# Optimization experiments

Hardware: AMD Instinct MI355X
Metric: run time of the kernel (lower is better)

## Reference

```python
import jax, jax.numpy as jnp
import numpy as np

EPS = 1e-6

def layernorm2d(x, w, b):
    # x: [B,C,H,W]; normalize over channel dim per spatial location
    mu = jnp.mean(x, axis=1, keepdims=True)
    var = jnp.var(x, axis=1, keepdims=True)
    xn = (x - mu) / jnp.sqrt(var + EPS)
    return xn * w[None, :, None, None] + b[None, :, None, None]

def mish(x):
    return x * jnp.tanh(jax.nn.softplus(x))

def setup_inputs() -> dict:
    key = jax.random.key(0)
    ks = jax.random.split(key, 16)
    B, C, H, W, T = 16, 192, 96, 96, 512
    s = 0.02
    return {
        "t": jax.random.normal(ks[0], (B, T), jnp.float32),
        "x_l": jax.random.normal(ks[1], (B, C, H, W), jnp.float32),
        "x_r": jax.random.normal(ks[2], (B, C, H, W), jnp.float32),
        "ln_wl": jnp.ones((C,), jnp.float32),
        "ln_bl": jnp.zeros((C,), jnp.float32),
        "ln_wr": jnp.ones((C,), jnp.float32),
        "ln_br": jnp.zeros((C,), jnp.float32),
        "Wl1": jax.random.normal(ks[3], (C, C), jnp.float32) * s,
        "bl1": jnp.zeros((C,), jnp.float32),
        "Wr1": jax.random.normal(ks[4], (C, C), jnp.float32) * s,
        "br1": jnp.zeros((C,), jnp.float32),
        "Wl2": jax.random.normal(ks[5], (C, C), jnp.float32) * s,
        "bl2": jnp.zeros((C,), jnp.float32),
        "Wr2": jax.random.normal(ks[6], (C, C), jnp.float32) * s,
        "br2": jnp.zeros((C,), jnp.float32),
        "beta": jnp.zeros((C,), jnp.float32),
        "gamma": jnp.zeros((C,), jnp.float32),
        "Wt": jax.random.normal(ks[7], (C, T), jnp.float32) * s,
        "bt": jnp.zeros((C,), jnp.float32),
    }

def reference(t, x_l, x_r, ln_wl, ln_bl, ln_wr, ln_br,
              Wl1, bl1, Wr1, br1, Wl2, bl2, Wr2, br2,
              beta, gamma, Wt, bt):
    C = x_l.shape[1]
    scale = C ** (-0.5)
    # 1x1 convs as channel einsums; outputs in bhwc layout
    Q_l = jnp.einsum('bchw,oc->bhwo', layernorm2d(x_l, ln_wl, ln_bl), Wl1) + bl1  # [B,H,Wl,C]
    Q_r = jnp.einsum('bchw,oc->bhwo', layernorm2d(x_r, ln_wr, ln_br), Wr1) + br1  # [B,H,Wr,C]
    V_l = jnp.einsum('bchw,oc->bhwo', x_l, Wl2) + bl2
    V_r = jnp.einsum('bchw,oc->bhwo', x_r, Wr2) + br2
    att = jnp.einsum('bhxc,bhyc->bhxy', Q_l, Q_r) * scale  # [B,H,Wl,Wr]
    F_r2l = jnp.einsum('bhxy,bhyc->bhxc', jax.nn.softmax(att, axis=-1), V_r)
    F_l2r = jnp.einsum('bhxy,bhxc->bhyc', jax.nn.softmax(att, axis=2), V_l)
    temb = (mish(t) @ Wt.T + bt)[:, :, None, None]  # [B,C,1,1]
    out_l = x_l + jnp.transpose(F_r2l, (0, 3, 1, 2)) * beta[None, :, None, None] + temb
    out_r = x_r + jnp.transpose(F_l2r, (0, 3, 1, 2)) * gamma[None, :, None, None] + temb
    return (out_l, out_r)
```

## Files before the change

kernel.cpp:

```cpp
#include <hip/hip_runtime.h>


typedef __attribute__((ext_vector_type(8))) short bhalf8;
typedef __attribute__((ext_vector_type(4))) float f32x4;

#define DEVI static __device__ __forceinline__

constexpr int Cc   = 192;
constexpr int HWc  = 9216;
constexpr int CHW  = 192 * 9216;
constexpr int HALF_OUT = 16 * CHW;

DEVI unsigned short f2bf(float f) {
  unsigned u = __builtin_bit_cast(unsigned, f);
  u += 0x7fffu + ((u >> 16) & 1u);
  return (unsigned short)(u >> 16);
}
DEVI float bf2f(unsigned short h) {
  unsigned u = (unsigned)h << 16;
  return __builtin_bit_cast(float, u);
}
DEVI float bf2f_s(short h) { return bf2f((unsigned short)h); }

__global__ void setup1(
    const float* __restrict__ t,
    const float* __restrict__ lnwl, const float* __restrict__ lnbl,
    const float* __restrict__ lnwr, const float* __restrict__ lnbr,
    const float* __restrict__ Wl1, const float* __restrict__ bl1,
    const float* __restrict__ Wr1, const float* __restrict__ br1,
    const float* __restrict__ Wl2, const float* __restrict__ Wr2,
    short* __restrict__ W1l_b, short* __restrict__ W1r_b,
    short* __restrict__ W2l_b, short* __restrict__ W2r_b,
    float* __restrict__ s1l, float* __restrict__ t1l,
    float* __restrict__ s1r, float* __restrict__ t1r,
    float* __restrict__ mt)
{
  const int blk = blockIdx.x, tid = threadIdx.x;
  if (blk < 576) {
    int id  = blk * 256 + tid;
    int m   = id / 36864;
    int rem = id - m * 36864;
    int c   = rem % 192;
    float v;
    short* dst;
    if (m == 0)      { v = lnwl[c] * Wl1[rem]; dst = W1l_b; }
    else if (m == 1) { v = lnwr[c] * Wr1[rem]; dst = W1r_b; }
    else if (m == 2) { v = Wl2[rem];           dst = W2l_b; }
    else             { v = Wr2[rem];           dst = W2r_b; }
    dst[rem] = (short)f2bf(v);
  } else if (blk == 576 || blk == 577) {
    if (tid < 192) {
      const float* Wm = (blk == 576) ? Wl1 : Wr1;
      const float* lw = (blk == 576) ? lnwl : lnwr;
      const float* lb = (blk == 576) ? lnbl : lnbr;
      const float* bb = (blk == 576) ? bl1 : br1;
      float s = 0.f, tb = 0.f;
      for (int c = 0; c < 192; ++c) {
        float wv = Wm[tid * 192 + c];
        s  += lw[c] * wv;
        tb += lb[c] * wv;
      }
      if (blk == 576) { s1l[tid] = s; t1l[tid] = tb + bb[tid]; }
      else            { s1r[tid] = s; t1r[tid] = tb + bb[tid]; }
    }
  } else {
    int id = (blk - 578) * 256 + tid;
    float v = t[id];
    float sp = (v > 20.f) ? v : log1pf(__expf(v));
    mt[id] = v * tanhf(sp);
  }
}

__global__ void setup2(const float* __restrict__ mt, const float* __restrict__ Wt,
                       const float* __restrict__ bt, float* __restrict__ temb)
{
  int id = blockIdx.x * 256 + threadIdx.x;
  int b = id / 192, o = id - b * 192;
  float s = 0.f;
  for (int k = 0; k < 512; ++k) s += mt[b * 512 + k] * Wt[o * 512 + k];
  temb[id] = s + bt[o];
}

struct SmemT {
  short buf1[96 * 200];
  short buf2[96 * 200];
  short vtl[192 * 96];
  short vtr[192 * 96];
  float misc[2112];
};
static_assert(sizeof(SmemT) <= 163840, "LDS overflow");

__launch_bounds__(768, 3)
__global__ void scam_main(
    const float* __restrict__ x_l, const float* __restrict__ x_r,
    const float* __restrict__ bl2, const float* __restrict__ br2,
    const float* __restrict__ beta, const float* __restrict__ gamma,
    const short* __restrict__ W1l_b, const short* __restrict__ W1r_b,
    const short* __restrict__ W2l_b, const short* __restrict__ W2r_b,
    const float* __restrict__ s1l, const float* __restrict__ t1l,
    const float* __restrict__ s1r, const float* __restrict__ t1r,
    const float* __restrict__ temb,
    float* __restrict__ out)
{
  __shared__ SmemT sm;
  const int tid  = threadIdx.x;
  const int lane = tid & 63;
  const int wid  = tid >> 6;
  const int m16  = lane & 15;
  const int kc8  = (lane >> 4) * 8;
  const int r4   = (lane >> 4) * 4;
  const int slice = blockIdx.x;
  const int bb_ = slice / 96;
  const int hh_ = slice - bb_ * 96;
  const int sliceBase = bb_ * CHW + hh_ * 96;

  for (int idx = tid; idx < 1728; idx += 768) {
    int a = idx / 192, o = idx - a * 192;
    switch (a) {
      case 0: sm.misc[1536 + o] = temb[bb_ * 192 + o]; break;
      case 1: sm.misc[384 + o]  = s1l[o]; break;
      case 2: sm.misc[576 + o]  = t1l[o]; break;
      case 3: sm.misc[768 + o]  = s1r[o]; break;
      case 4: sm.misc[960 + o]  = t1r[o]; break;
      case 5: sm.misc[1152 + o] = bl2[o]; break;
      case 6: sm.misc[1344 + o] = br2[o]; break;
      case 7: sm.misc[1728 + o] = beta[o]; break;
      default: sm.misc[1920 + o] = gamma[o]; break;
    }
  }

  #pragma unroll
  for (int j = 0; j < 6; ++j) {
    int i4 = j * 768 + tid;
    int c  = i4 / 24;
    int w4 = i4 - c * 24;
    const float4 xl4 = *reinterpret_cast<const float4*>(x_l + sliceBase + c * HWc + w4 * 4);
    const float4 xr4 = *reinterpret_cast<const float4*>(x_r + sliceBase + c * HWc + w4 * 4);
    int base = w4 * 4 * 200 + c;
    sm.buf1[base      ] = (short)f2bf(xl4.x);
    sm.buf1[base + 200] = (short)f2bf(xl4.y);
    sm.buf1[base + 400] = (short)f2bf(xl4.z);
    sm.buf1[base + 600] = (short)f2bf(xl4.w);
    sm.buf2[base      ] = (short)f2bf(xr4.x);
    sm.buf2[base + 200] = (short)f2bf(xr4.y);
    sm.buf2[base + 400] = (short)f2bf(xr4.z);
    sm.buf2[base + 600] = (short)f2bf(xr4.w);
  }
  __syncthreads();

  {
    int side = (tid >= 384) ? 1 : 0;
    int rest = tid - side * 384;
    int w = rest >> 2;
    int q = rest & 3;
    const short* Xb = side ? sm.buf2 : sm.buf1;
    float s0 = 0.f, s2 = 0.f;
    #pragma unroll
    for (int mc = 0; mc < 6; ++mc) {
      bhalf8 v = *reinterpret_cast<const bhalf8*>(Xb + w * 200 + q * 48 + mc * 8);
      #pragma unroll
      for (int e = 0; e < 8; ++e) { float f = bf2f_s(v[e]); s0 += f; s2 += f * f; }
    }
    s0 += __shfl_xor(s0, 1); s2 += __shfl_xor(s2, 1);
    s0 += __shfl_xor(s0, 2); s2 += __shfl_xor(s2, 2);
    if (q == 0) {
      float mu  = s0 * (1.f / 192.f);
      float var = s2 * (1.f / 192.f) - mu * mu;
      float rs  = rsqrtf(var + 1e-6f);
      sm.misc[side * 192 + w]      = mu;
      sm.misc[side * 192 + 96 + w] = rs;
    }
  }
  __syncthreads();

  #pragma unroll
  for (int sd = 0; sd < 2; ++sd) {
    const short* Wb = sd ? W2r_b : W2l_b;
    const short* Xb = sd ? sm.buf2 : sm.buf1;
    short* Vt = sd ? sm.vtr : sm.vtl;
    const float* bv = sm.misc + 1152 + sd * 192;
    const int crow = wid * 16 + m16;
    bhalf8 af[6];
    #pragma unroll
    for (int k = 0; k < 6; ++k)
      af[k] = *reinterpret_cast<const bhalf8*>(Wb + crow * 192 + k * 32 + kc8);
    #pragma unroll
    for (int xi = 0; xi < 6; ++xi) {
      f32x4 acc = {0.f, 0.f, 0.f, 0.f};
      #pragma unroll
      for (int k = 0; k < 6; ++k) {
        bhalf8 bfr = *reinterpret_cast<const bhalf8*>(Xb + (xi * 16 + m16) * 200 + k * 32 + kc8);
        acc = __builtin_amdgcn_mfma_f32_16x16x32_bf16(af[k], bfr, acc, 0, 0, 0);
      }
      const int xcol = xi * 16 + m16;
      #pragma unroll
      for (int j = 0; j < 4; ++j) {
        int cr = wid * 16 + r4 + j;
        Vt[cr * 96 + xcol] = (short)f2bf(acc[j] + bv[cr]);
      }
    }
  }

  f32x4 accQ0[6], accQ1[6];
  {
    const int orow = wid * 16 + m16;
    {
      bhalf8 bfq[6];
      #pragma unroll
      for (int k = 0; k < 6; ++k)
        bfq[k] = *reinterpret_cast<const bhalf8*>(W1l_b + orow * 192 + k * 32 + kc8);
      #pragma unroll
      for (int mi = 0; mi < 6; ++mi) {
        f32x4 acc = {0.f, 0.f, 0.f, 0.f};
        #pragma unroll
        for (int k = 0; k < 6; ++k) {
          bhalf8 afr = *reinterpret_cast<const bhalf8*>(sm.buf1 + (mi * 16 + m16) * 200 + k * 32 + kc8);
          acc = __builtin_amdgcn_mfma_f32_16x16x32_bf16(afr, bfq[k], acc, 0, 0, 0);
        }
        accQ0[mi] = acc;
      }
    }
    {
      bhalf8 bfq[6];
      #pragma unroll
      for (int k = 0; k < 6; ++k)
        bfq[k] = *reinterpret_cast<const bhalf8*>(W1r_b + orow * 192 + k * 32 + kc8);
      #pragma unroll
      for (int mi = 0; mi < 6; ++mi) {
        f32x4 acc = {0.f, 0.f, 0.f, 0.f};
        #pragma unroll
        for (int k = 0; k < 6; ++k) {
          bhalf8 afr = *reinterpret_cast<const bhalf8*>(sm.buf2 + (mi * 16 + m16) * 200 + k * 32 + kc8);
          acc = __builtin_amdgcn_mfma_f32_16x16x32_bf16(afr, bfq[k], acc, 0, 0, 0);
        }
        accQ1[mi] = acc;
      }
    }
  }
  __syncthreads();
  {
    const int o = wid * 16 + m16;
    #pragma unroll
    for (int sd = 0; sd < 2; ++sd) {
      short* Qb = sd ? sm.buf2 : sm.buf1;
      const float* muA = sm.misc + sd * 192;
      const float* rsA = muA + 96;
      float s1o = sm.misc[384 + sd * 384 + o];
      float t1o = sm.misc[576 + sd * 384 + o];
      #pragma unroll
      for (int mi = 0; mi < 6; ++mi) {
        f32x4 acc = sd ? accQ1[mi] : accQ0[mi];
        #pragma unroll
        for (int j = 0; j < 4; ++j) {
          int x = mi * 16 + r4 + j;
          float mu = muA[x], rs = rsA[x];
          Qb[x * 200 + o] = (short)f2bf(rs * acc[j] - mu * rs * s1o + t1o);
        }
      }
    }
  }
  __syncthreads();

  {
    const int mi = wid >> 1;
    const int yb = (wid & 1) * 3;
    bhalf8 afa[6];
    #pragma unroll
    for (int k = 0; k < 6; ++k)
      afa[k] = *reinterpret_cast<const bhalf8*>(sm.buf1 + (mi * 16 + m16) * 200 + k * 32 + kc8);
    f32x4 accA[3];
    #pragma unroll
    for (int yt = 0; yt < 3; ++yt) {
      f32x4 acc = {0.f, 0.f, 0.f, 0.f};
      #pragma unroll
      for (int k = 0; k < 6; ++k) {
        bhalf8 bfy = *reinterpret_cast<const bhalf8*>(sm.buf2 + ((yb + yt) * 16 + m16) * 200 + k * 32 + kc8);
        acc = __builtin_amdgcn_mfma_f32_16x16x32_bf16(afa[k], bfy, acc, 0, 0, 0);
      }
      accA[yt] = acc;
    }
    __syncthreads();
    float* attf = reinterpret_cast<float*>(sm.buf1);
    const float scale = 0.07216878364870323f;
    #pragma unroll
    for (int yt = 0; yt < 3; ++yt) {
      #pragma unroll
      for (int j = 0; j < 4; ++j) {
        int x = mi * 16 + r4 + j;
        int y = (yb + yt) * 16 + m16;
        attf[x * 96 + (y ^ (x & 31))] = accA[yt][j] * scale;
      }
    }
  }
  __syncthreads();

  {
    const float* attf = reinterpret_cast<const float*>(sm.buf1);
    short* Pr = sm.buf2;
    short* Pc = sm.buf2 + 9216;
    const int r = tid >> 3;
    const int p = tid & 7;
    {
      float av[12];
      #pragma unroll
      for (int k = 0; k < 12; ++k)
        av[k] = attf[r * 96 + ((p * 12 + k) ^ (r & 31))];
      float mx = av[0];
      #pragma unroll
      for (int k = 1; k < 12; ++k) mx = fmaxf(mx, av[k]);
      mx = fmaxf(mx, __shfl_xor(mx, 1));
      mx = fmaxf(mx, __shfl_xor(mx, 2));
      mx = fmaxf(mx, __shfl_xor(mx, 4));
      float s = 0.f;
      #pragma unroll
      for (int k = 0; k < 12; ++k) { av[k] = __expf(av[k] - mx); s += av[k]; }
      s += __shfl_xor(s, 1); s += __shfl_xor(s, 2); s += __shfl_xor(s, 4);
      float inv = 1.f / s;
      #pragma unroll
      for (int k = 0; k < 12; k += 2) {
        unsigned u = (unsigned)f2bf(av[k] * inv) | ((unsigned)f2bf(av[k + 1] * inv) << 16);
        *reinterpret_cast<unsigned*>(Pr + r * 96 + p * 12 + k) = u;
      }
    }
    {
      float av[12];
      #pragma unroll
      for (int k = 0; k < 12; ++k) {
        int x = p * 12 + k;
        av[k] = attf[x * 96 + (r ^ (x & 31))];
      }
      float mx = av[0];
      #pragma unroll
      for (int k = 1; k < 12; ++k) mx = fmaxf(mx, av[k]);
      mx = fmaxf(mx, __shfl_xor(mx, 1));
      mx = fmaxf(mx, __shfl_xor(mx, 2));
      mx = fmaxf(mx, __shfl_xor(mx, 4));
      float s = 0.f;
      #pragma unroll
      for (int k = 0; k < 12; ++k) { av[k] = __expf(av[k] - mx); s += av[k]; }
      s += __shfl_xor(s, 1); s += __shfl_xor(s, 2); s += __shfl_xor(s, 4);
      float inv = 1.f / s;
      #pragma unroll
      for (int k = 0; k < 12; k += 2) {
        unsigned u = (unsigned)f2bf(av[k] * inv) | ((unsigned)f2bf(av[k + 1] * inv) << 16);
        *reinterpret_cast<unsigned*>(Pc + r * 96 + p * 12 + k) = u;
      }
    }
  }
  __syncthreads();

  f32x4 accF[6], accG[6];
  {
    const short* Pr = sm.buf2;
    const short* Pc = sm.buf2 + 9216;
    const int crow = wid * 16 + m16;
    bhalf8 vf[3], vg[3];
    #pragma unroll
    for (int k = 0; k < 3; ++k) {
      vf[k] = *reinterpret_cast<const bhalf8*>(sm.vtr + crow * 96 + k * 32 + kc8);
      vg[k] = *reinterpret_cast<const bhalf8*>(sm.vtl + crow * 96 + k * 32 + kc8);
    }
    #pragma unroll
    for (int xi = 0; xi < 6; ++xi) {
      f32x4 a1 = {0.f, 0.f, 0.f, 0.f}, a2 = {0.f, 0.f, 0.f, 0.f};
      #pragma unroll
      for (int k = 0; k < 3; ++k) {
        bhalf8 ap = *reinterpret_cast<const bhalf8*>(Pr + (xi * 16 + m16) * 96 + k * 32 + kc8);
        a1 = __builtin_amdgcn_mfma_f32_16x16x32_bf16(ap, vf[k], a1, 0, 0, 0);
        bhalf8 aq = *reinterpret_cast<const bhalf8*>(Pc + (xi * 16 + m16) * 96 + k * 32 + kc8);
        a2 = __builtin_amdgcn_mfma_f32_16x16x32_bf16(aq, vg[k], a2, 0, 0, 0);
      }
      accF[xi] = a1; accG[xi] = a2;
    }
  }
  __syncthreads();
  {
    const int cc2 = wid * 16 + m16;
    #pragma unroll
    for (int xi = 0; xi < 6; ++xi) {
      #pragma unroll
      for (int j = 0; j < 4; ++j) {
        int x = xi * 16 + r4 + j;
        sm.buf1[x * 200 + cc2] = (short)f2bf(accF[xi][j]);
        sm.buf2[x * 200 + cc2] = (short)f2bf(accG[xi][j]);
      }
    }
  }
  __syncthreads();

  #pragma unroll
  for (int sd = 0; sd < 2; ++sd) {
    const float* xg = sd ? x_r : x_l;
    float* og = out + (sd ? HALF_OUT : 0);
    const short* Fb = sd ? sm.buf2 : sm.buf1;
    const float* coef = sm.misc + (sd ? 1920 : 1728);
    #pragma unroll
    for (int j = 0; j < 6; ++j) {
      int i4 = j * 768 + tid;
      int c  = i4 / 24;
      int w4 = i4 - c * 24;
      const float4 xv = *reinterpret_cast<const float4*>(xg + sliceBase + c * HWc + w4 * 4);
      float cf = coef[c];
      float tv = sm.misc[1536 + c];
      int fb = w4 * 4 * 200 + c;
      float4 ov;
      ov.x = xv.x + bf2f_s(Fb[fb      ]) * cf + tv;
      ov.y = xv.y + bf2f_s(Fb[fb + 200]) * cf + tv;
      ov.z = xv.z + bf2f_s(Fb[fb + 400]) * cf + tv;
      ov.w = xv.w + bf2f_s(Fb[fb + 600]) * cf + tv;
      *reinterpret_cast<float4*>(og + sliceBase + c * HWc + w4 * 4) = ov;
    }
  }
}

extern "C" void kernel_launch(void* const* d_in, const int* in_sizes, int n_in,
                              void* d_out, int out_size, void* d_ws, size_t ws_size,
                              hipStream_t stream)
{
  const float* t    = (const float*)d_in[0];
  const float* x_l  = (const float*)d_in[1];
  const float* x_r  = (const float*)d_in[2];
  const float* lnwl = (const float*)d_in[3];
  const float* lnbl = (const float*)d_in[4];
  const float* lnwr = (const float*)d_in[5];
  const float* lnbr = (const float*)d_in[6];
  const float* Wl1  = (const float*)d_in[7];
  const float* bl1  = (const float*)d_in[8];
  const float* Wr1  = (const float*)d_in[9];
  const float* br1  = (const float*)d_in[10];
  const float* Wl2  = (const float*)d_in[11];
  const float* bl2  = (const float*)d_in[12];
  const float* Wr2  = (const float*)d_in[13];
  const float* br2  = (const float*)d_in[14];
  const float* beta = (const float*)d_in[15];
  const float* gamma= (const float*)d_in[16];
  const float* Wt   = (const float*)d_in[17];
  const float* bt   = (const float*)d_in[18];
  float* out = (float*)d_out;

  char* ws = (char*)d_ws;
  short* W1l_b = (short*)ws;
  short* W1r_b = W1l_b + 36864;
  short* W2l_b = W1r_b + 36864;
  short* W2r_b = W2l_b + 36864;
  float* fws  = (float*)(ws + 4 * 73728);
  float* s1l  = fws;
  float* t1l  = fws + 192;
  float* s1r  = fws + 384;
  float* t1r  = fws + 576;
  float* temb = fws + 768;
  float* mt   = fws + 3840;

  setup1<<<610, 256, 0, stream>>>(t, lnwl, lnbl, lnwr, lnbr, Wl1, bl1, Wr1, br1,
                                  Wl2, Wr2, W1l_b, W1r_b, W2l_b, W2r_b,
                                  s1l, t1l, s1r, t1r, mt);
  setup2<<<12, 256, 0, stream>>>(mt, Wt, bt, temb);
  scam_main<<<1536, 768, 0, stream>>>(x_l, x_r, bl2, br2, beta, gamma,
                                      W1l_b, W1r_b, W2l_b, W2r_b,
                                      s1l, t1l, s1r, t1r, temb, out);
}
```

Measured before the change: 285.5 us.

## Pad LDS strides, keep per-channel params in registers, hoist Q weight loads, drop sync

Pads the V-transpose and softmax-probability LDS arrays to a 104-element stride to cut bank conflicts on the MFMA fragment reads. Per-channel affine and bias values are loaded straight into registers instead of staged through LDS, which shrinks the misc area. The Q-projection weight fragments are loaded before the first barrier so their global latency overlaps the input staging, and the barrier between the stats pass and the V projection is removed. The load/store index order is swapped so consecutive threads walk channels rather than width. That spreads LDS writes across banks but makes the global float4 accesses strided by HW, hurting coalescing.

```diff
diff --git a/kernel.cpp b/kernel.cpp
--- a/kernel.cpp
+++ b/kernel.cpp
@@ -10,6 +10,7 @@
 constexpr int HWc  = 9216;
 constexpr int CHW  = 192 * 9216;
 constexpr int HALF_OUT = 16 * CHW;
+constexpr int PS   = 104;
 
 DEVI unsigned short f2bf(float f) {
   unsigned u = __builtin_bit_cast(unsigned, f);
@@ -83,10 +84,10 @@
 
 struct SmemT {
   short buf1[96 * 200];
-  short buf2[96 * 200];
-  short vtl[192 * 96];
-  short vtr[192 * 96];
-  float misc[2112];
+  short buf2[19968];
+  short vtl[192 * PS];
+  short vtr[192 * PS];
+  float misc[960];
 };
 static_assert(sizeof(SmemT) <= 163840, "LDS overflow");
 
@@ -113,30 +114,32 @@
   const int bb_ = slice / 96;
   const int hh_ = slice - bb_ * 96;
   const int sliceBase = bb_ * CHW + hh_ * 96;
-
-  for (int idx = tid; idx < 1728; idx += 768) {
-    int a = idx / 192, o = idx - a * 192;
-    switch (a) {
-      case 0: sm.misc[1536 + o] = temb[bb_ * 192 + o]; break;
-      case 1: sm.misc[384 + o]  = s1l[o]; break;
-      case 2: sm.misc[576 + o]  = t1l[o]; break;
-      case 3: sm.misc[768 + o]  = s1r[o]; break;
-      case 4: sm.misc[960 + o]  = t1r[o]; break;
-      case 5: sm.misc[1152 + o] = bl2[o]; break;
-      case 6: sm.misc[1344 + o] = br2[o]; break;
-      case 7: sm.misc[1728 + o] = beta[o]; break;
-      default: sm.misc[1920 + o] = gamma[o]; break;
-    }
+  const int o_wm = wid * 16 + m16;
+
+  float s1Lr = s1l[o_wm], t1Lr = t1l[o_wm];
+  float s1Rr = s1r[o_wm], t1Rr = t1r[o_wm];
+  float bvL[4], bvR[4];
+  #pragma unroll
+  for (int j = 0; j < 4; ++j) {
+    bvL[j] = bl2[wid * 16 + r4 + j];
+    bvR[j] = br2[wid * 16 + r4 + j];
+  }
+
+  if (tid < 576) {
+    int a = tid / 192, o = tid - a * 192;
+    if (a == 0)      sm.misc[384 + o] = temb[bb_ * 192 + o];
+    else if (a == 1) sm.misc[576 + o] = beta[o];
+    else             sm.misc[768 + o] = gamma[o];
   }
 
   #pragma unroll
   for (int j = 0; j < 6; ++j) {
     int i4 = j * 768 + tid;
-    int c  = i4 / 24;
-    int w4 = i4 - c * 24;
-    const float4 xl4 = *reinterpret_cast<const float4*>(x_l + sliceBase + c * HWc + w4 * 4);
-    const float4 xr4 = *reinterpret_cast<const float4*>(x_r + sliceBase + c * HWc + w4 * 4);
-    int base = w4 * 4 * 200 + c;
+    int wq = i4 / 192;
+    int c  = i4 - wq * 192;
+    const float4 xl4 = *reinterpret_cast<const float4*>(x_l + sliceBase + c * HWc + wq * 4);
+    const float4 xr4 = *reinterpret_cast<const float4*>(x_r + sliceBase + c * HWc + wq * 4);
+    int base = wq * 4 * 200 + c;
     sm.buf1[base      ] = (short)f2bf(xl4.x);
     sm.buf1[base + 200] = (short)f2bf(xl4.y);
     sm.buf1[base + 400] = (short)f2bf(xl4.z);
@@ -146,6 +149,13 @@
     sm.buf2[base + 400] = (short)f2bf(xr4.z);
     sm.buf2[base + 600] = (short)f2bf(xr4.w);
   }
+
+  bhalf8 bfqL[6], bfqR[6];
+  #pragma unroll
+  for (int k = 0; k < 6; ++k) {
+    bfqL[k] = *reinterpret_cast<const bhalf8*>(W1l_b + o_wm * 192 + k * 32 + kc8);
+    bfqR[k] = *reinterpret_cast<const bhalf8*>(W1r_b + o_wm * 192 + k * 32 + kc8);
+  }
   __syncthreads();
 
   {
@@ -171,19 +181,17 @@
       sm.misc[side * 192 + 96 + w] = rs;
     }
   }
-  __syncthreads();
 
   #pragma unroll
   for (int sd = 0; sd < 2; ++sd) {
     const short* Wb = sd ? W2r_b : W2l_b;
     const short* Xb = sd ? sm.buf2 : sm.buf1;
     short* Vt = sd ? sm.vtr : sm.vtl;
-    const float* bv = sm.misc + 1152 + sd * 192;
-    const int crow = wid * 16 + m16;
+    const float* bv = sd ? bvR : bvL;
     bhalf8 af[6];
     #pragma unroll
     for (int k = 0; k < 6; ++k)
-      af[k] = *reinterpret_cast<const bhalf8*>(Wb + crow * 192 + k * 32 + kc8);
+      af[k] = *reinterpret_cast<const bhalf8*>(Wb + o_wm * 192 + k * 32 + kc8);
     #pragma unroll
     for (int xi = 0; xi < 6; ++xi) {
       f32x4 acc = {0.f, 0.f, 0.f, 0.f};
@@ -196,57 +204,44 @@
       #pragma unroll
       for (int j = 0; j < 4; ++j) {
         int cr = wid * 16 + r4 + j;
-        Vt[cr * 96 + xcol] = (short)f2bf(acc[j] + bv[cr]);
+        Vt[cr * PS + xcol] = (short)f2bf(acc[j] + bv[j]);
       }
     }
   }
 
   f32x4 accQ0[6], accQ1[6];
   {
-    const int orow = wid * 16 + m16;
-    {
-      bhalf8 bfq[6];
-      #pragma unroll
-      for (int k = 0; k < 6; ++k)
-        bfq[k] = *reinterpret_cast<const bhalf8*>(W1l_b + orow * 192 + k * 32 + kc8);
-      #pragma unroll
-      for (int mi = 0; mi < 6; ++mi) {
-        f32x4 acc = {0.f, 0.f, 0.f, 0.f};
-        #pragma unroll
-        for (int k = 0; k < 6; ++k) {
-          bhalf8 afr = *reinterpret_cast<const bhalf8*>(sm.buf1 + (mi * 16 + m16) * 200 + k * 32 + kc8);
-          acc = __builtin_amdgcn_mfma_f32_16x16x32_bf16(afr, bfq[k], acc, 0, 0, 0);
-        }
-        accQ0[mi] = acc;
-      }
-    }
-    {
-      bhalf8 bfq[6];
-      #pragma unroll
-      for (int k = 0; k < 6; ++k)
-        bfq[k] = *reinterpret_cast<const bhalf8*>(W1r_b + orow * 192 + k * 32 + kc8);
-      #pragma unroll
-      for (int mi = 0; mi < 6; ++mi) {
-        f32x4 acc = {0.f, 0.f, 0.f, 0.f};
-        #pragma unroll
-        for (int k = 0; k < 6; ++k) {
-          bhalf8 afr = *reinterpret_cast<const bhalf8*>(sm.buf2 + (mi * 16 + m16) * 200 + k * 32 + kc8);
-          acc = __builtin_amdgcn_mfma_f32_16x16x32_bf16(afr, bfq[k], acc, 0, 0, 0);
-        }
-        accQ1[mi] = acc;
-      }
-    }
-  }
-  __syncthreads();
-  {
-    const int o = wid * 16 + m16;
+    #pragma unroll
+    for (int mi = 0; mi < 6; ++mi) {
+      f32x4 acc = {0.f, 0.f, 0.f, 0.f};
+      #pragma unroll
+      for (int k = 0; k < 6; ++k) {
+        bhalf8 afr = *reinterpret_cast<const bhalf8*>(sm.buf1 + (mi * 16 + m16) * 200 + k * 32 + kc8);
+        acc = __builtin_amdgcn_mfma_f32_16x16x32_bf16(afr, bfqL[k], acc, 0, 0, 0);
+      }
+      accQ0[mi] = acc;
+    }
+    #pragma unroll
+    for (int mi = 0; mi < 6; ++mi) {
+      f32x4 acc = {0.f, 0.f, 0.f, 0.f};
+      #pragma unroll
+      for (int k = 0; k < 6; ++k) {
+        bhalf8 afr = *reinterpret_cast<const bhalf8*>(sm.buf2 + (mi * 16 + m16) * 200 + k * 32 + kc8);
+        acc = __builtin_amdgcn_mfma_f32_16x16x32_bf16(afr, bfqR[k], acc, 0, 0, 0);
+      }
+      accQ1[mi] = acc;
+    }
+  }
+  __syncthreads();
+  {
+    const int o = o_wm;
     #pragma unroll
     for (int sd = 0; sd < 2; ++sd) {
       short* Qb = sd ? sm.buf2 : sm.buf1;
       const float* muA = sm.misc + sd * 192;
       const float* rsA = muA + 96;
-      float s1o = sm.misc[384 + sd * 384 + o];
-      float t1o = sm.misc[576 + sd * 384 + o];
+      float s1o = sd ? s1Rr : s1Lr;
+      float t1o = sd ? t1Rr : t1Lr;
       #pragma unroll
       for (int mi = 0; mi < 6; ++mi) {
         f32x4 acc = sd ? accQ1[mi] : accQ0[mi];
@@ -297,7 +292,7 @@
   {
     const float* attf = reinterpret_cast<const float*>(sm.buf1);
     short* Pr = sm.buf2;
-    short* Pc = sm.buf2 + 9216;
+    short* Pc = sm.buf2 + 96 * PS;
     const int r = tid >> 3;
     const int p = tid & 7;
     {
@@ -319,7 +314,7 @@
       #pragma unroll
       for (int k = 0; k < 12; k += 2) {
         unsigned u = (unsigned)f2bf(av[k] * inv) | ((unsigned)f2bf(av[k + 1] * inv) << 16);
-        *reinterpret_cast<unsigned*>(Pr + r * 96 + p * 12 + k) = u;
+        *reinterpret_cast<unsigned*>(Pr + r * PS + p * 12 + k) = u;
       }
     }
     {
@@ -343,7 +338,7 @@
       #pragma unroll
       for (int k = 0; k < 12; k += 2) {
         unsigned u = (unsigned)f2bf(av[k] * inv) | ((unsigned)f2bf(av[k + 1] * inv) << 16);
-        *reinterpret_cast<unsigned*>(Pc + r * 96 + p * 12 + k) = u;
+        *reinterpret_cast<unsigned*>(Pc + r * PS + p * 12 + k) = u;
       }
     }
   }
@@ -352,22 +347,21 @@
   f32x4 accF[6], accG[6];
   {
     const short* Pr = sm.buf2;
-    const short* Pc = sm.buf2 + 9216;
-    const int crow = wid * 16 + m16;
+    const short* Pc = sm.buf2 + 96 * PS;
     bhalf8 vf[3], vg[3];
     #pragma unroll
     for (int k = 0; k < 3; ++k) {
-      vf[k] = *reinterpret_cast<const bhalf8*>(sm.vtr + crow * 96 + k * 32 + kc8);
-      vg[k] = *reinterpret_cast<const bhalf8*>(sm.vtl + crow * 96 + k * 32 + kc8);
+      vf[k] = *reinterpret_cast<const bhalf8*>(sm.vtr + o_wm * PS + k * 32 + kc8);
+      vg[k] = *reinterpret_cast<const bhalf8*>(sm.vtl + o_wm * PS + k * 32 + kc8);
     }
     #pragma unroll
     for (int xi = 0; xi < 6; ++xi) {
       f32x4 a1 = {0.f, 0.f, 0.f, 0.f}, a2 = {0.f, 0.f, 0.f, 0.f};
       #pragma unroll
       for (int k = 0; k < 3; ++k) {
-        bhalf8 ap = *reinterpret_cast<const bhalf8*>(Pr + (xi * 16 + m16) * 96 + k * 32 + kc8);
+        bhalf8 ap = *reinterpret_cast<const bhalf8*>(Pr + (xi * 16 + m16) * PS + k * 32 + kc8);
         a1 = __builtin_amdgcn_mfma_f32_16x16x32_bf16(ap, vf[k], a1, 0, 0, 0);
-        bhalf8 aq = *reinterpret_cast<const bhalf8*>(Pc + (xi * 16 + m16) * 96 + k * 32 + kc8);
+        bhalf8 aq = *reinterpret_cast<const bhalf8*>(Pc + (xi * 16 + m16) * PS + k * 32 + kc8);
         a2 = __builtin_amdgcn_mfma_f32_16x16x32_bf16(aq, vg[k], a2, 0, 0, 0);
       }
       accF[xi] = a1; accG[xi] = a2;
@@ -375,7 +369,7 @@
   }
   __syncthreads();
   {
-    const int cc2 = wid * 16 + m16;
+    const int cc2 = o_wm;
     #pragma unroll
     for (int xi = 0; xi < 6; ++xi) {
       #pragma unroll
@@ -393,22 +387,22 @@
     const float* xg = sd ? x_r : x_l;
     float* og = out + (sd ? HALF_OUT : 0);
     const short* Fb = sd ? sm.buf2 : sm.buf1;
-    const float* coef = sm.misc + (sd ? 1920 : 1728);
+    const float* coef = sm.misc + (sd ? 768 : 576);
     #pragma unroll
     for (int j = 0; j < 6; ++j) {
       int i4 = j * 768 + tid;
-      int c  = i4 / 24;
-      int w4 = i4 - c * 24;
-      const float4 xv = *reinterpret_cast<const float4*>(xg + sliceBase + c * HWc + w4 * 4);
+      int wq = i4 / 192;
+      int c  = i4 - wq * 192;
+      const float4 xv = *reinterpret_cast<const float4*>(xg + sliceBase + c * HWc + wq * 4);
       float cf = coef[c];
-      float tv = sm.misc[1536 + c];
-      int fb = w4 * 4 * 200 + c;
+      float tv = sm.misc[384 + c];
+      int fb = wq * 4 * 200 + c;
       float4 ov;
       ov.x = xv.x + bf2f_s(Fb[fb      ]) * cf + tv;
       ov.y = xv.y + bf2f_s(Fb[fb + 200]) * cf + tv;
       ov.z = xv.z + bf2f_s(Fb[fb + 400]) * cf + tv;
       ov.w = xv.w + bf2f_s(Fb[fb + 600]) * cf + tv;
-      *reinterpret_cast<float4*>(og + sliceBase + c * HWc + w4 * 4) = ov;
+      *reinterpret_cast<float4*>(og + sliceBase + c * HWc + wq * 4) = ov;
     }
   }
 }
```

Result: slower. 472.6 us (+65.5%).
